# Performance work log

Hardware: AMD Instinct MI355X
Metric: run time of the kernel (lower is better)

Reference implementation:

```python
import jax, jax.numpy as jnp
import numpy as np

B, SEQ_LEN, PRED_LEN, LABEL_LEN, PERIOD, N_CH = 32, 2048, 1024, 512, 256, 256
K = SEQ_LEN // PERIOD   # seg_num_x = 8
L = PRED_LEN // PERIOD  # seg_num_y = 4
EPS = 1e-5


def setup_inputs() -> dict:
    key = jax.random.key(0)
    k1, k2, k3, k4, k5, k6, k7 = jax.random.split(key, 7)
    x_enc = jax.random.normal(k1, (B, SEQ_LEN, N_CH), jnp.float32)
    x_mark_enc = jax.random.normal(k2, (B, SEQ_LEN, 4), jnp.float32)
    x_dec = jax.random.normal(k3, (B, LABEL_LEN + PRED_LEN, N_CH), jnp.float32)
    x_mark_dec = jax.random.normal(k4, (B, LABEL_LEN + PRED_LEN, 4), jnp.float32)
    # base_model abstracted as a linear map on the time axis of a [B, PERIOD, N] segment.
    # Scaled ~1/sqrt(P) so repeated powers (up to K+L-1 = 11) stay numerically tame.
    W_base = jax.random.normal(k5, (PERIOD, PERIOD), jnp.float32) * (0.9 / np.sqrt(PERIOD))
    # new_encoders[j]: nn.Linear(seg_num_x, 1) -> weight row [K] + bias scalar per j.
    W_enc = jax.random.normal(k6, (L, K), jnp.float32) * (1.0 / np.sqrt(K))
    b_enc = jax.random.normal(k7, (L,), jnp.float32) * 0.01
    return {"x_enc": x_enc, "x_mark_enc": x_mark_enc, "x_dec": x_dec,
            "x_mark_dec": x_mark_dec, "W_base": W_base, "W_enc": W_enc, "b_enc": b_enc}


def reference(x_enc, x_mark_enc, x_dec, x_mark_dec, W_base, W_enc, b_enc):
    Bv, S, N = x_enc.shape
    # per-series normalization over time (means is .detach()'d in torch; fwd math identical)
    means = jnp.mean(x_enc, axis=1, keepdims=True)                  # [B,1,N]
    xc = x_enc - means
    stdev = jnp.sqrt(jnp.var(xc, axis=1, keepdims=True) + EPS)      # [B,1,N]
    xn = xc / stdev

    # split into K segments of length PERIOD: [K, B, P, N]
    segs = xn.reshape(Bv, K, PERIOD, N).transpose(1, 0, 2, 3)

    # x_res[l][k] = base_model applied (K - k + l) times to segment k.
    # base(x) = einsum('qp,bpn->bqn', W_base, x), so m applications = W_base^m.
    def step(c, _):
        nxt = W_base @ c
        return nxt, nxt
    _, rest = jax.lax.scan(step, W_base, None, length=K + L - 2)
    powers = jnp.concatenate([W_base[None], rest], axis=0)          # powers[i] = W^(i+1)

    exps = (K - jnp.arange(K))[None, :] + jnp.arange(L)[:, None]    # [L,K]
    Wlk = powers[exps - 1]                                          # [L,K,P,P]
    x_res = jnp.einsum('lkqp,kbpn->lkbqn', Wlk, segs)               # [L,K,B,P,N]

    # dec_out_part[l] = sum_k W_enc[l,k] * x_res[l][k] + b_enc[l] * ones
    dec = jnp.einsum('lk,lkbqn->lbqn', W_enc, x_res) + b_enc[:, None, None, None]
    dec = dec.transpose(1, 0, 2, 3).reshape(Bv, L * PERIOD, N)      # cat over time

    # de-normalize
    dec = dec * stdev[:, 0, :][:, None, :] + means[:, 0, :][:, None, :]
    return dec[:, -PRED_LEN:, :]
```

## Files before the change

### kernel.cpp

```cpp
#include <hip/hip_runtime.h>
#include <cstdint>
#include <cstddef>


typedef unsigned short ushort_t;
typedef unsigned int uint_t;
typedef __attribute__((ext_vector_type(8))) short bf16x8;
typedef __attribute__((ext_vector_type(16))) float f32x16;

__device__ __forceinline__ ushort_t f32_to_bf16(float f) {
    uint_t u = __float_as_uint(f);
    u += 0x7FFFu + ((u >> 16) & 1u);
    return (ushort_t)(u >> 16);
}
__device__ __forceinline__ float bf16_to_f32(ushort_t h) {
    return __uint_as_float((uint_t)h << 16);
}

struct PowOps { int sa[4]; int sb[4]; int sd[4]; };

__global__ void powmul(const float* __restrict__ Wb, float* __restrict__ Pw, PowOps ops) {
    __shared__ float As[4 * 256];
    const int mat = blockIdx.x;
    const int r0  = blockIdx.y * 4;
    const int tid = threadIdx.x;
    const float* A  = (ops.sa[mat] < 0) ? Wb : Pw + (size_t)ops.sa[mat] * 65536;
    const float* Bm = (ops.sb[mat] < 0) ? Wb : Pw + (size_t)ops.sb[mat] * 65536;
    float* C        = Pw + (size_t)ops.sd[mat] * 65536;
#pragma unroll
    for (int i = 0; i < 4; ++i) As[i * 256 + tid] = A[(size_t)(r0 + i) * 256 + tid];
    __syncthreads();
    float a0 = 0.f, a1 = 0.f, a2 = 0.f, a3 = 0.f;
    for (int p = 0; p < 256; p += 8) {
        float bv[8];
#pragma unroll
        for (int u = 0; u < 8; ++u) bv[u] = Bm[(size_t)(p + u) * 256 + tid];
#pragma unroll
        for (int u = 0; u < 8; ++u) {
            a0 += As[0 * 256 + p + u] * bv[u];
            a1 += As[1 * 256 + p + u] * bv[u];
            a2 += As[2 * 256 + p + u] * bv[u];
            a3 += As[3 * 256 + p + u] * bv[u];
        }
    }
    C[(size_t)(r0 + 0) * 256 + tid] = a0;
    C[(size_t)(r0 + 1) * 256 + tid] = a1;
    C[(size_t)(r0 + 2) * 256 + tid] = a2;
    C[(size_t)(r0 + 3) * 256 + tid] = a3;
}

__global__ void prep(const float* __restrict__ x, ushort_t* __restrict__ Xt,
                     float* __restrict__ ps1, float* __restrict__ ps2,
                     const float* __restrict__ Pw, const float* __restrict__ Wb,
                     const float* __restrict__ Wenc,
                     ushort_t* __restrict__ Ah, float* __restrict__ rsA) {
    __shared__ float lds[64 * 65];
    __shared__ float red1[16 * 64];
    __shared__ float red2[16 * 64];
    const int bid = blockIdx.x;
    const int tid = threadIdx.x;
    if (bid < 4096) {
        const int st = bid & 31;
        const int nt = (bid >> 5) & 3;
        const int b  = bid >> 7;
        const int c = tid & 15, r = tid >> 4;
        const int s0 = st * 64;
        float s1[4] = {0,0,0,0}, s2[4] = {0,0,0,0};
#pragma unroll
        for (int it = 0; it < 4; ++it) {
            const int ii = r + it * 16;
            const float4 v = *(const float4*)(x + ((size_t)b * 2048 + s0 + ii) * 256 + nt * 64 + c * 4);
            const float vv[4] = {v.x, v.y, v.z, v.w};
#pragma unroll
            for (int jj = 0; jj < 4; ++jj) {
                lds[ii * 65 + c * 4 + jj] = vv[jj];
                s1[jj] += vv[jj]; s2[jj] += vv[jj] * vv[jj];
            }
        }
#pragma unroll
        for (int jj = 0; jj < 4; ++jj) { red1[r * 64 + c * 4 + jj] = s1[jj]; red2[r * 64 + c * 4 + jj] = s2[jj]; }
        __syncthreads();
        if (tid < 64) {
            float a = 0.f, q = 0.f;
#pragma unroll
            for (int rr = 0; rr < 16; ++rr) { a += red1[rr * 64 + tid]; q += red2[rr * 64 + tid]; }
            const size_t o = (size_t)st * 8192 + b * 256 + nt * 64 + tid;
            ps1[o] = a; ps2[o] = q;
        }
#pragma unroll
        for (int step = 0; step < 8; ++step) {
            const int npr = step * 8 + (tid >> 5);
            const int sp  = (tid & 31) * 2;
            const float f0 = lds[sp * 65 + npr];
            const float f1 = lds[(sp + 1) * 65 + npr];
            const uint_t packed = (uint_t)f32_to_bf16(f0) | ((uint_t)f32_to_bf16(f1) << 16);
            *(uint_t*)(Xt + ((size_t)b * 256 + nt * 64 + npr) * 2048 + s0 + sp) = packed;
        }
    } else {
        const int t = bid - 4096;
        const int l = t >> 8, q = t & 255;
        const int c = tid;
        float part = 0.f;
#pragma unroll
        for (int k = 0; k < 8; ++k) {
            const int m = 8 - k + l;
            const float* src = (m == 1) ? Wb : (Pw + (size_t)(m - 2) * 65536);
            const float val = Wenc[l * 8 + k] * src[q * 256 + c];
            const ushort_t h = f32_to_bf16(val);
            Ah[(size_t)t * 2048 + k * 256 + c] = h;
            part += bf16_to_f32(h);
        }
#pragma unroll
        for (int off = 32; off > 0; off >>= 1) part += __shfl_xor(part, off);
        if ((c & 63) == 0) red1[c >> 6] = part;
        __syncthreads();
        if (c == 0) rsA[t] = red1[0] + red1[1] + red1[2] + red1[3];
    }
}

#define GLOAD_LDS16(gsrc, ldst) \
    __builtin_amdgcn_global_load_lds((const __attribute__((address_space(1))) void*)(gsrc), \
                                     (__attribute__((address_space(3))) void*)(ldst), 16, 0, 0)

__global__ __launch_bounds__(256, 2) void gemm_kernel(
    const ushort_t* __restrict__ Ah,
    const ushort_t* __restrict__ Xt,
    const float* __restrict__ ps1, const float* __restrict__ ps2,
    const float* __restrict__ rsA, const float* __restrict__ benc,
    float* __restrict__ out)
{
    __shared__ ushort_t sA[3][4096];
    __shared__ ushort_t sX[3][4096];

    const int flat = blockIdx.x;
    const int xcd  = flat & 7;
    const int j    = flat >> 3;
    const int bx   = xcd + ((j & 7) << 3);
    const int by   = j >> 3;
    const int l    = by >> 1;

    const int tid  = threadIdx.x;
    const int lane = tid & 63;
    const int w    = tid >> 6;
    const int wm   = w >> 1, wn = w & 1;
    const int li   = lane & 31, lg = lane >> 5;
    const int lq3  = (li >> 1) & 3;

    const int lrow = 2 * (lane >> 3) + ((lane >> 2) & 1);
    const int kc   = (lane & 3) ^ ((lane >> 3) & 3);
    const ushort_t* aBase0 = Ah + (size_t)(by * 128 + 16 * (2 * w + 0) + lrow) * 2048 + kc * 8;
    const ushort_t* aBase1 = Ah + (size_t)(by * 128 + 16 * (2 * w + 1) + lrow) * 2048 + kc * 8;
    const ushort_t* xBase0 = Xt + (size_t)(bx * 128 + 16 * (2 * w + 0) + lrow) * 2048 + kc * 8;
    const ushort_t* xBase1 = Xt + (size_t)(bx * 128 + 16 * (2 * w + 1) + lrow) * 2048 + kc * 8;

    ushort_t* sAf = &sA[0][0];
    ushort_t* sXf = &sX[0][0];

#define STAGE(dst_off, ko_) do { \
    GLOAD_LDS16(aBase0 + (ko_), sAf + (dst_off) + (2 * w + 0) * 512); \
    GLOAD_LDS16(aBase1 + (ko_), sAf + (dst_off) + (2 * w + 1) * 512); \
    GLOAD_LDS16(xBase0 + (ko_), sXf + (dst_off) + (2 * w + 0) * 512); \
    GLOAD_LDS16(xBase1 + (ko_), sXf + (dst_off) + (2 * w + 1) * 512); \
} while (0)

    f32x16 acc[2][2];
#pragma unroll
    for (int mm = 0; mm < 2; ++mm)
#pragma unroll
        for (int nn = 0; nn < 2; ++nn)
#pragma unroll
            for (int rr = 0; rr < 16; ++rr) acc[mm][nn][rr] = 0.0f;

    STAGE(0, 0);
    STAGE(4096, 32);

    int cb = 0;
#pragma unroll 1
    for (int kt = 0; kt < 64; ++kt) {
        if (kt < 63) { asm volatile("s_waitcnt vmcnt(4)" ::: "memory"); }
        else         { asm volatile("s_waitcnt vmcnt(0)" ::: "memory"); }
        __builtin_amdgcn_s_barrier();
        asm volatile("" ::: "memory");

        const ushort_t* pa = sAf + cb * 4096;
        const ushort_t* px = sXf + cb * 4096;
        bf16x8 af[2][2], xf[2][2];
#pragma unroll
        for (int ks = 0; ks < 2; ++ks) {
            const int sl = ((ks << 1) + lg) ^ lq3;
            const int ro = (li >> 1) * 64 + (li & 1) * 32 + sl * 8;
            af[ks][0] = *(const bf16x8*)(pa + wm * 2048 + ro);
            af[ks][1] = *(const bf16x8*)(pa + wm * 2048 + 1024 + ro);
            xf[ks][0] = *(const bf16x8*)(px + wn * 2048 + ro);
            xf[ks][1] = *(const bf16x8*)(px + wn * 2048 + 1024 + ro);
        }
        if (kt < 62) {
            const int sb_ = (cb >= 1) ? cb - 1 : 2;
            STAGE(sb_ * 4096, (kt + 2) * 32);
        }
        __builtin_amdgcn_s_setprio(1);
#pragma unroll
        for (int ks = 0; ks < 2; ++ks) {
            acc[0][0] = __builtin_amdgcn_mfma_f32_32x32x16_bf16(af[ks][0], xf[ks][0], acc[0][0], 0, 0, 0);
            acc[0][1] = __builtin_amdgcn_mfma_f32_32x32x16_bf16(af[ks][0], xf[ks][1], acc[0][1], 0, 0, 0);
            acc[1][0] = __builtin_amdgcn_mfma_f32_32x32x16_bf16(af[ks][1], xf[ks][0], acc[1][0], 0, 0, 0);
            acc[1][1] = __builtin_amdgcn_mfma_f32_32x32x16_bf16(af[ks][1], xf[ks][1], acc[1][1], 0, 0, 0);
        }
        __builtin_amdgcn_s_setprio(0);
        asm volatile("" ::: "memory");
        cb = (cb == 2) ? 0 : cb + 1;
    }
#undef STAGE

    const float be = benc[l];
    float mn[2], sd[2];
#pragma unroll
    for (int nn = 0; nn < 2; ++nn) {
        const int col = bx * 128 + wn * 64 + nn * 32 + li;
        float s = 0.f, q = 0.f;
#pragma unroll
        for (int st = 0; st < 32; ++st) {
            s += ps1[(size_t)st * 8192 + col];
            q += ps2[(size_t)st * 8192 + col];
        }
        const float mean = s * (1.0f / 2048.0f);
        float var = q * (1.0f / 2048.0f) - mean * mean;
        var = fmaxf(var, 0.0f);
        mn[nn] = mean;
        sd[nn] = sqrtf(var + 1e-5f);
    }
#pragma unroll
    for (int mm = 0; mm < 2; ++mm)
#pragma unroll
        for (int nn = 0; nn < 2; ++nn) {
            const int col = bx * 128 + wn * 64 + nn * 32 + li;
            const int bq = col >> 8, nq = col & 255;
            const float ben = be * sd[nn];
#pragma unroll
            for (int rr = 0; rr < 16; ++rr) {
                const int row = by * 128 + wm * 64 + mm * 32 + ((rr & 3) + 8 * (rr >> 2) + 4 * lg);
                out[((size_t)bq * 1024 + row) * 256 + nq] =
                    acc[mm][nn][rr] + mn[nn] * (1.0f - rsA[row]) + ben;
            }
        }
}

extern "C" void kernel_launch(void* const* d_in, const int* in_sizes, int n_in,
                              void* d_out, int out_size, void* d_ws, size_t ws_size,
                              hipStream_t stream) {
    (void)in_sizes; (void)n_in; (void)out_size; (void)ws_size;
    const float* x_enc  = (const float*)d_in[0];
    const float* W_base = (const float*)d_in[4];
    const float* W_enc  = (const float*)d_in[5];
    const float* b_enc  = (const float*)d_in[6];
    float* out = (float*)d_out;

    char* ws = (char*)d_ws;
    float*    wsP   = (float*)(ws);
    float*    wsRsA = (float*)(ws + 0x300000);
    float*    wsS1  = (float*)(ws + 0x310000);
    float*    wsS2  = (float*)(ws + 0x410000);
    ushort_t* wsAh  = (ushort_t*)(ws + 0x510000);
    ushort_t* wsXt  = (ushort_t*)(ws + 0x910000);

    { PowOps o{{-1, 0, 0, 0}, {-1, 0, 0, 0}, {0, 0, 0, 0}};
      powmul<<<dim3(1, 64), 256, 0, stream>>>(W_base, wsP, o); }
    { PowOps o{{0, 0, 0, 0}, {-1, 0, 0, 0}, {1, 2, 0, 0}};
      powmul<<<dim3(2, 64), 256, 0, stream>>>(W_base, wsP, o); }
    { PowOps o{{2, 2, 2, 2}, {-1, 0, 1, 2}, {3, 4, 5, 6}};
      powmul<<<dim3(4, 64), 256, 0, stream>>>(W_base, wsP, o); }
    { PowOps o{{6, 6, 6, 0}, {-1, 0, 1, 0}, {7, 8, 9, 0}};
      powmul<<<dim3(3, 64), 256, 0, stream>>>(W_base, wsP, o); }

    prep<<<5120, 256, 0, stream>>>(x_enc, wsXt, wsS1, wsS2, wsP, W_base, W_enc,
                                   wsAh, wsRsA);

    gemm_kernel<<<512, 256, 0, stream>>>(wsAh, wsXt, wsS1, wsS2, wsRsA, b_enc, out);
}
```

Baseline: 106.8 us.

## Factor weight powers to shrink the GEMM reduction and add a combine stage

The single large GEMM (reduction length 2048 over all segments) is replaced with a factored form W^(8-k+l) = W^l · W^(8-k). First V_k = W^(8-k)·x_k is computed per segment, then a combine kernel mixes the V_k with W_enc per output segment, and a second GEMM applies W^l (identity for l=0). This cuts total MAC work by about 2.7x and drops the highest matrix-power launch. In exchange it writes and re-reads large bf16 intermediates, adds a kernel launch, and rounds to bf16 two extra times, which risks accuracy. Mean/std finalisation and the row-sum correction move into extra blocks of the first GEMM.

```diff
diff --git a/kernel.cpp b/kernel.cpp
--- a/kernel.cpp
+++ b/kernel.cpp
@@ -52,8 +52,7 @@
 __global__ void prep(const float* __restrict__ x, ushort_t* __restrict__ Xt,
                      float* __restrict__ ps1, float* __restrict__ ps2,
                      const float* __restrict__ Pw, const float* __restrict__ Wb,
-                     const float* __restrict__ Wenc,
-                     ushort_t* __restrict__ Ah, float* __restrict__ rsA) {
+                     ushort_t* __restrict__ Pb, float* __restrict__ prs) {
     __shared__ float lds[64 * 65];
     __shared__ float red1[16 * 64];
     __shared__ float red2[16 * 64];
@@ -97,24 +96,42 @@
             *(uint_t*)(Xt + ((size_t)b * 256 + nt * 64 + npr) * 2048 + s0 + sp) = packed;
         }
     } else {
-        const int t = bid - 4096;
-        const int l = t >> 8, q = t & 255;
-        const int c = tid;
-        float part = 0.f;
-#pragma unroll
-        for (int k = 0; k < 8; ++k) {
-            const int m = 8 - k + l;
-            const float* src = (m == 1) ? Wb : (Pw + (size_t)(m - 2) * 65536);
-            const float val = Wenc[l * 8 + k] * src[q * 256 + c];
-            const ushort_t h = f32_to_bf16(val);
-            Ah[(size_t)t * 2048 + k * 256 + c] = h;
-            part += bf16_to_f32(h);
-        }
-#pragma unroll
-        for (int off = 32; off > 0; off >>= 1) part += __shfl_xor(part, off);
-        if ((c & 63) == 0) red1[c >> 6] = part;
-        __syncthreads();
-        if (c == 0) rsA[t] = red1[0] + red1[1] + red1[2] + red1[3];
+        const int ib = bid - 4096;
+        const int e  = ib >> 2;
+        const int rq = ib & 3;
+        const int q  = rq * 64 + (tid >> 2);
+        const int cc = tid & 3;
+        uint2* dst = (uint2*)(Pb + (size_t)e * 65536 + q * 256 + cc * 64);
+        float s = 0.f;
+        if (e == 0) {
+#pragma unroll
+            for (int i = 0; i < 16; ++i) {
+                uint2 o; o.x = 0u; o.y = 0u;
+                const int col0 = cc * 64 + i * 4;
+                if (q >= col0 && q < col0 + 4) {
+                    const int j = q - col0;
+                    if (j == 0) o.x = 0x3F80u; else if (j == 1) o.x = 0x3F800000u;
+                    else if (j == 2) o.y = 0x3F80u; else o.y = 0x3F800000u;
+                }
+                dst[i] = o;
+            }
+            s = 1.0f;
+        } else {
+            const float* src = (e == 1) ? Wb : (Pw + (size_t)(e - 2) * 65536);
+            const float4* sp = (const float4*)(src + (size_t)q * 256 + cc * 64);
+#pragma unroll
+            for (int i = 0; i < 16; ++i) {
+                const float4 v = sp[i];
+                const ushort_t h0 = f32_to_bf16(v.x), h1 = f32_to_bf16(v.y);
+                const ushort_t h2 = f32_to_bf16(v.z), h3 = f32_to_bf16(v.w);
+                s += bf16_to_f32(h0) + bf16_to_f32(h1) + bf16_to_f32(h2) + bf16_to_f32(h3);
+                uint2 o; o.x = (uint_t)h0 | ((uint_t)h1 << 16); o.y = (uint_t)h2 | ((uint_t)h3 << 16);
+                dst[i] = o;
+            }
+        }
+        s += __shfl_xor(s, 1);
+        s += __shfl_xor(s, 2);
+        if (cc == 0) prs[e * 256 + q] = s;
     }
 }
 
@@ -122,22 +139,191 @@
     __builtin_amdgcn_global_load_lds((const __attribute__((address_space(1))) void*)(gsrc), \
                                      (__attribute__((address_space(3))) void*)(ldst), 16, 0, 0)
 
-__global__ __launch_bounds__(256, 2) void gemm_kernel(
-    const ushort_t* __restrict__ Ah,
+__global__ __launch_bounds__(256, 2) void gemm_v(
+    const ushort_t* __restrict__ Pb,
     const ushort_t* __restrict__ Xt,
+    ushort_t* __restrict__ vt,
     const float* __restrict__ ps1, const float* __restrict__ ps2,
+    const float* __restrict__ prs, const float* __restrict__ Wenc,
+    float* __restrict__ meanv, float* __restrict__ stdv, float* __restrict__ rsA)
+{
+    __shared__ ushort_t sAa[3][4096];
+    __shared__ ushort_t sBb[3][8192];
+
+    const int bid = blockIdx.x;
+    const int tid = threadIdx.x;
+    if (bid >= 512) {
+        const int idx = bid - 512;
+        if (idx < 32) {
+            const int b = idx;
+            float s = 0.f, q = 0.f;
+#pragma unroll
+            for (int st = 0; st < 32; ++st) {
+                s += ps1[(size_t)st * 8192 + b * 256 + tid];
+                q += ps2[(size_t)st * 8192 + b * 256 + tid];
+            }
+            const float mean = s * (1.0f / 2048.0f);
+            float var = q * (1.0f / 2048.0f) - mean * mean;
+            var = fmaxf(var, 0.0f);
+            meanv[b * 256 + tid] = mean;
+            stdv [b * 256 + tid] = sqrtf(var + 1e-5f);
+        } else {
+            const int l = idx - 32;
+            float u = 0.f;
+#pragma unroll
+            for (int k = 0; k < 8; ++k) u += Wenc[l * 8 + k] * prs[(8 - k) * 256 + tid];
+            float* uf = (float*)&sAa[0][0];
+            uf[tid] = u;
+            __syncthreads();
+            const uint2* rp = (const uint2*)(Pb + (size_t)l * 65536 + tid * 256);
+            float s = 0.f;
+#pragma unroll
+            for (int i = 0; i < 64; ++i) {
+                const uint2 v = rp[i];
+                s += bf16_to_f32((ushort_t)(v.x & 0xffff)) * uf[i * 4 + 0]
+                   + bf16_to_f32((ushort_t)(v.x >> 16))    * uf[i * 4 + 1]
+                   + bf16_to_f32((ushort_t)(v.y & 0xffff)) * uf[i * 4 + 2]
+                   + bf16_to_f32((ushort_t)(v.y >> 16))    * uf[i * 4 + 3];
+            }
+            rsA[l * 256 + tid] = s;
+        }
+        return;
+    }
+
+    const int xcd  = bid & 7;
+    const int g    = bid >> 3;
+    const int colT = xcd + ((g & 7) << 3);
+    const int k    = g >> 3;
+    const int e    = 8 - k;
+
+    const int lane = tid & 63;
+    const int w    = tid >> 6;
+    const int wm   = w >> 1, wn = w & 1;
+    const int li   = lane & 31, lg = lane >> 5;
+    const int lq3  = (li >> 1) & 3;
+    const int lrow = 2 * (lane >> 3) + ((lane >> 2) & 1);
+    const int kc   = (lane & 3) ^ ((lane >> 3) & 3);
+
+    const ushort_t* xtb = Xt + (size_t)(colT * 128) * 2048 + k * 256;
+    const ushort_t* pbb = Pb + (size_t)e * 65536;
+
+#define VSTAGE(bf_, kt_) do { \
+    const int p0_ = (kt_) * 32 + kc * 8; \
+    GLOAD_LDS16(xtb + (size_t)(w * 32 + 0  + lrow) * 2048 + p0_, &sAa[bf_][(w * 32 + 0)  * 32]); \
+    GLOAD_LDS16(xtb + (size_t)(w * 32 + 16 + lrow) * 2048 + p0_, &sAa[bf_][(w * 32 + 16) * 32]); \
+    GLOAD_LDS16(pbb + (w * 64 + 0  + lrow) * 256 + p0_, &sBb[bf_][(w * 64 + 0)  * 32]); \
+    GLOAD_LDS16(pbb + (w * 64 + 16 + lrow) * 256 + p0_, &sBb[bf_][(w * 64 + 16) * 32]); \
+    GLOAD_LDS16(pbb + (w * 64 + 32 + lrow) * 256 + p0_, &sBb[bf_][(w * 64 + 32) * 32]); \
+    GLOAD_LDS16(pbb + (w * 64 + 48 + lrow) * 256 + p0_, &sBb[bf_][(w * 64 + 48) * 32]); \
+} while (0)
+
+    f32x16 acc[2][4];
+#pragma unroll
+    for (int mm = 0; mm < 2; ++mm)
+#pragma unroll
+        for (int nn = 0; nn < 4; ++nn)
+#pragma unroll
+            for (int rr = 0; rr < 16; ++rr) acc[mm][nn][rr] = 0.0f;
+
+    VSTAGE(0, 0);
+    VSTAGE(1, 1);
+
+#define VKT(kt_) do { \
+    if ((kt_) < 7) { asm volatile("s_waitcnt vmcnt(6)" ::: "memory"); } \
+    else           { asm volatile("s_waitcnt vmcnt(0)" ::: "memory"); } \
+    __builtin_amdgcn_s_barrier(); \
+    asm volatile("" ::: "memory"); \
+    const ushort_t* pa_ = &sAa[(kt_) % 3][0]; \
+    const ushort_t* px_ = &sBb[(kt_) % 3][0]; \
+    bf16x8 af[2][2], xf[2][4]; \
+    _Pragma("unroll") \
+    for (int ks = 0; ks < 2; ++ks) { \
+        const int sl = ((ks << 1) + lg) ^ lq3; \
+        const int ro = (li >> 1) * 64 + (li & 1) * 32 + sl * 8; \
+        af[ks][0] = *(const bf16x8*)(pa_ + wm * 2048 + ro); \
+        af[ks][1] = *(const bf16x8*)(pa_ + wm * 2048 + 1024 + ro); \
+        xf[ks][0] = *(const bf16x8*)(px_ + wn * 4096 + ro); \
+        xf[ks][1] = *(const bf16x8*)(px_ + wn * 4096 + 1024 + ro); \
+        xf[ks][2] = *(const bf16x8*)(px_ + wn * 4096 + 2048 + ro); \
+        xf[ks][3] = *(const bf16x8*)(px_ + wn * 4096 + 3072 + ro); \
+    } \
+    if ((kt_) < 6) { VSTAGE(((kt_) + 2) % 3, (kt_) + 2); } \
+    __builtin_amdgcn_s_setprio(1); \
+    _Pragma("unroll") \
+    for (int ks = 0; ks < 2; ++ks) \
+        _Pragma("unroll") \
+        for (int mm = 0; mm < 2; ++mm) \
+            _Pragma("unroll") \
+            for (int nn = 0; nn < 4; ++nn) \
+                acc[mm][nn] = __builtin_amdgcn_mfma_f32_32x32x16_bf16(af[ks][mm], xf[ks][nn], acc[mm][nn], 0, 0, 0); \
+    __builtin_amdgcn_s_setprio(0); \
+    asm volatile("" ::: "memory"); \
+} while (0)
+
+    VKT(0); VKT(1); VKT(2); VKT(3); VKT(4); VKT(5); VKT(6); VKT(7);
+#undef VKT
+#undef VSTAGE
+
+    ushort_t* vb = vt + (size_t)k * 2097152;
+#pragma unroll
+    for (int mm = 0; mm < 2; ++mm)
+#pragma unroll
+        for (int nn = 0; nn < 4; ++nn) {
+            const int q = wn * 128 + nn * 32 + li;
+#pragma unroll
+            for (int rr = 0; rr < 16; ++rr) {
+                const int c = colT * 128 + wm * 64 + mm * 32 + ((rr & 3) + 8 * (rr >> 2) + 4 * lg);
+                vb[(size_t)c * 256 + q] = f32_to_bf16(acc[mm][nn][rr]);
+            }
+        }
+}
+
+__global__ void combine(const ushort_t* __restrict__ vt, const float* __restrict__ Wenc,
+                        ushort_t* __restrict__ c) {
+    const int t   = threadIdx.x;
+    const int col = blockIdx.x * 8 + (t >> 5);
+    const size_t off = (size_t)col * 256 + (t & 31) * 8;
+    float a0[8] = {0,0,0,0,0,0,0,0}, a1[8] = {0,0,0,0,0,0,0,0};
+    float a2[8] = {0,0,0,0,0,0,0,0}, a3[8] = {0,0,0,0,0,0,0,0};
+#pragma unroll
+    for (int k = 0; k < 8; ++k) {
+        const bf16x8 v = *(const bf16x8*)(vt + (size_t)k * 2097152 + off);
+        const float w0 = Wenc[0 * 8 + k], w1 = Wenc[1 * 8 + k];
+        const float w2 = Wenc[2 * 8 + k], w3 = Wenc[3 * 8 + k];
+#pragma unroll
+        for (int j = 0; j < 8; ++j) {
+            const float f = bf16_to_f32((ushort_t)v[j]);
+            a0[j] += w0 * f; a1[j] += w1 * f; a2[j] += w2 * f; a3[j] += w3 * f;
+        }
+    }
+    bf16x8 o0, o1, o2, o3;
+#pragma unroll
+    for (int j = 0; j < 8; ++j) {
+        o0[j] = (short)f32_to_bf16(a0[j]); o1[j] = (short)f32_to_bf16(a1[j]);
+        o2[j] = (short)f32_to_bf16(a2[j]); o3[j] = (short)f32_to_bf16(a3[j]);
+    }
+    *(bf16x8*)(c + 0 * 2097152 + off) = o0;
+    *(bf16x8*)(c + 1 * 2097152 + off) = o1;
+    *(bf16x8*)(c + 2 * 2097152 + off) = o2;
+    *(bf16x8*)(c + 3 * 2097152 + off) = o3;
+}
+
+__global__ __launch_bounds__(256, 2) void gemm2(
+    const ushort_t* __restrict__ Pb, const ushort_t* __restrict__ c,
+    const float* __restrict__ meanv, const float* __restrict__ stdv,
     const float* __restrict__ rsA, const float* __restrict__ benc,
     float* __restrict__ out)
 {
-    __shared__ ushort_t sA[3][4096];
-    __shared__ ushort_t sX[3][4096];
-
-    const int flat = blockIdx.x;
-    const int xcd  = flat & 7;
-    const int j    = flat >> 3;
-    const int bx   = xcd + ((j & 7) << 3);
-    const int by   = j >> 3;
-    const int l    = by >> 1;
+    __shared__ ushort_t sAa[3][4096];
+    __shared__ ushort_t sBb[3][4096];
+
+    const int bid  = blockIdx.x;
+    const int xcd  = bid & 7;
+    const int g    = bid >> 3;
+    const int colT = xcd + ((g & 7) << 3);
+    const int rest = g >> 3;
+    const int l    = rest >> 1;
+    const int qpT  = rest & 1;
 
     const int tid  = threadIdx.x;
     const int lane = tid & 63;
@@ -145,22 +331,18 @@
     const int wm   = w >> 1, wn = w & 1;
     const int li   = lane & 31, lg = lane >> 5;
     const int lq3  = (li >> 1) & 3;
-
     const int lrow = 2 * (lane >> 3) + ((lane >> 2) & 1);
     const int kc   = (lane & 3) ^ ((lane >> 3) & 3);
-    const ushort_t* aBase0 = Ah + (size_t)(by * 128 + 16 * (2 * w + 0) + lrow) * 2048 + kc * 8;
-    const ushort_t* aBase1 = Ah + (size_t)(by * 128 + 16 * (2 * w + 1) + lrow) * 2048 + kc * 8;
-    const ushort_t* xBase0 = Xt + (size_t)(bx * 128 + 16 * (2 * w + 0) + lrow) * 2048 + kc * 8;
-    const ushort_t* xBase1 = Xt + (size_t)(bx * 128 + 16 * (2 * w + 1) + lrow) * 2048 + kc * 8;
-
-    ushort_t* sAf = &sA[0][0];
-    ushort_t* sXf = &sX[0][0];
-
-#define STAGE(dst_off, ko_) do { \
-    GLOAD_LDS16(aBase0 + (ko_), sAf + (dst_off) + (2 * w + 0) * 512); \
-    GLOAD_LDS16(aBase1 + (ko_), sAf + (dst_off) + (2 * w + 1) * 512); \
-    GLOAD_LDS16(xBase0 + (ko_), sXf + (dst_off) + (2 * w + 0) * 512); \
-    GLOAD_LDS16(xBase1 + (ko_), sXf + (dst_off) + (2 * w + 1) * 512); \
+
+    const ushort_t* ab = Pb + (size_t)l * 65536 + (size_t)(qpT * 128) * 256;
+    const ushort_t* cb = c + ((size_t)l * 8192 + colT * 128) * 256;
+
+#define GSTAGE(bf_, kt_) do { \
+    const int p0_ = (kt_) * 32 + kc * 8; \
+    GLOAD_LDS16(ab + (w * 32 + 0  + lrow) * 256 + p0_, &sAa[bf_][(w * 32 + 0)  * 32]); \
+    GLOAD_LDS16(ab + (w * 32 + 16 + lrow) * 256 + p0_, &sAa[bf_][(w * 32 + 16) * 32]); \
+    GLOAD_LDS16(cb + (w * 32 + 0  + lrow) * 256 + p0_, &sBb[bf_][(w * 32 + 0)  * 32]); \
+    GLOAD_LDS16(cb + (w * 32 + 16 + lrow) * 256 + p0_, &sBb[bf_][(w * 32 + 16) * 32]); \
 } while (0)
 
     f32x16 acc[2][2];
@@ -171,76 +353,64 @@
 #pragma unroll
             for (int rr = 0; rr < 16; ++rr) acc[mm][nn][rr] = 0.0f;
 
-    STAGE(0, 0);
-    STAGE(4096, 32);
-
-    int cb = 0;
-#pragma unroll 1
-    for (int kt = 0; kt < 64; ++kt) {
-        if (kt < 63) { asm volatile("s_waitcnt vmcnt(4)" ::: "memory"); }
-        else         { asm volatile("s_waitcnt vmcnt(0)" ::: "memory"); }
-        __builtin_amdgcn_s_barrier();
-        asm volatile("" ::: "memory");
-
-        const ushort_t* pa = sAf + cb * 4096;
-        const ushort_t* px = sXf + cb * 4096;
-        bf16x8 af[2][2], xf[2][2];
-#pragma unroll
-        for (int ks = 0; ks < 2; ++ks) {
-            const int sl = ((ks << 1) + lg) ^ lq3;
-            const int ro = (li >> 1) * 64 + (li & 1) * 32 + sl * 8;
-            af[ks][0] = *(const bf16x8*)(pa + wm * 2048 + ro);
-            af[ks][1] = *(const bf16x8*)(pa + wm * 2048 + 1024 + ro);
-            xf[ks][0] = *(const bf16x8*)(px + wn * 2048 + ro);
-            xf[ks][1] = *(const bf16x8*)(px + wn * 2048 + 1024 + ro);
-        }
-        if (kt < 62) {
-            const int sb_ = (cb >= 1) ? cb - 1 : 2;
-            STAGE(sb_ * 4096, (kt + 2) * 32);
-        }
-        __builtin_amdgcn_s_setprio(1);
-#pragma unroll
-        for (int ks = 0; ks < 2; ++ks) {
-            acc[0][0] = __builtin_amdgcn_mfma_f32_32x32x16_bf16(af[ks][0], xf[ks][0], acc[0][0], 0, 0, 0);
-            acc[0][1] = __builtin_amdgcn_mfma_f32_32x32x16_bf16(af[ks][0], xf[ks][1], acc[0][1], 0, 0, 0);
-            acc[1][0] = __builtin_amdgcn_mfma_f32_32x32x16_bf16(af[ks][1], xf[ks][0], acc[1][0], 0, 0, 0);
-            acc[1][1] = __builtin_amdgcn_mfma_f32_32x32x16_bf16(af[ks][1], xf[ks][1], acc[1][1], 0, 0, 0);
-        }
-        __builtin_amdgcn_s_setprio(0);
-        asm volatile("" ::: "memory");
-        cb = (cb == 2) ? 0 : cb + 1;
-    }
-#undef STAGE
+    GSTAGE(0, 0);
+    GSTAGE(1, 1);
+
+#define GKT(kt_) do { \
+    if ((kt_) < 7) { asm volatile("s_waitcnt vmcnt(4)" ::: "memory"); } \
+    else           { asm volatile("s_waitcnt vmcnt(0)" ::: "memory"); } \
+    __builtin_amdgcn_s_barrier(); \
+    asm volatile("" ::: "memory"); \
+    const ushort_t* pa_ = &sAa[(kt_) % 3][0]; \
+    const ushort_t* px_ = &sBb[(kt_) % 3][0]; \
+    bf16x8 af[2][2], xf[2][2]; \
+    _Pragma("unroll") \
+    for (int ks = 0; ks < 2; ++ks) { \
+        const int sl = ((ks << 1) + lg) ^ lq3; \
+        const int ro = (li >> 1) * 64 + (li & 1) * 32 + sl * 8; \
+        af[ks][0] = *(const bf16x8*)(pa_ + wm * 2048 + ro); \
+        af[ks][1] = *(const bf16x8*)(pa_ + wm * 2048 + 1024 + ro); \
+        xf[ks][0] = *(const bf16x8*)(px_ + wn * 2048 + ro); \
+        xf[ks][1] = *(const bf16x8*)(px_ + wn * 2048 + 1024 + ro); \
+    } \
+    if ((kt_) < 6) { GSTAGE(((kt_) + 2) % 3, (kt_) + 2); } \
+    __builtin_amdgcn_s_setprio(1); \
+    _Pragma("unroll") \
+    for (int ks = 0; ks < 2; ++ks) { \
+        acc[0][0] = __builtin_amdgcn_mfma_f32_32x32x16_bf16(af[ks][0], xf[ks][0], acc[0][0], 0, 0, 0); \
+        acc[0][1] = __builtin_amdgcn_mfma_f32_32x32x16_bf16(af[ks][0], xf[ks][1], acc[0][1], 0, 0, 0); \
+        acc[1][0] = __builtin_amdgcn_mfma_f32_32x32x16_bf16(af[ks][1], xf[ks][0], acc[1][0], 0, 0, 0); \
+        acc[1][1] = __builtin_amdgcn_mfma_f32_32x32x16_bf16(af[ks][1], xf[ks][1], acc[1][1], 0, 0, 0); \
+    } \
+    __builtin_amdgcn_s_setprio(0); \
+    asm volatile("" ::: "memory"); \
+} while (0)
+
+    GKT(0); GKT(1); GKT(2); GKT(3); GKT(4); GKT(5); GKT(6); GKT(7);
+#undef GKT
+#undef GSTAGE
 
     const float be = benc[l];
     float mn[2], sd[2];
 #pragma unroll
     for (int nn = 0; nn < 2; ++nn) {
-        const int col = bx * 128 + wn * 64 + nn * 32 + li;
-        float s = 0.f, q = 0.f;
-#pragma unroll
-        for (int st = 0; st < 32; ++st) {
-            s += ps1[(size_t)st * 8192 + col];
-            q += ps2[(size_t)st * 8192 + col];
-        }
-        const float mean = s * (1.0f / 2048.0f);
-        float var = q * (1.0f / 2048.0f) - mean * mean;
-        var = fmaxf(var, 0.0f);
-        mn[nn] = mean;
-        sd[nn] = sqrtf(var + 1e-5f);
+        const int col = colT * 128 + wn * 64 + nn * 32 + li;
+        mn[nn] = meanv[col];
+        sd[nn] = stdv [col];
     }
 #pragma unroll
     for (int mm = 0; mm < 2; ++mm)
 #pragma unroll
         for (int nn = 0; nn < 2; ++nn) {
-            const int col = bx * 128 + wn * 64 + nn * 32 + li;
+            const int col = colT * 128 + wn * 64 + nn * 32 + li;
             const int bq = col >> 8, nq = col & 255;
             const float ben = be * sd[nn];
 #pragma unroll
             for (int rr = 0; rr < 16; ++rr) {
-                const int row = by * 128 + wm * 64 + mm * 32 + ((rr & 3) + 8 * (rr >> 2) + 4 * lg);
-                out[((size_t)bq * 1024 + row) * 256 + nq] =
-                    acc[mm][nn][rr] + mn[nn] * (1.0f - rsA[row]) + ben;
+                const int trow = l * 256 + qpT * 128 + wm * 64 + mm * 32
+                               + ((rr & 3) + 8 * (rr >> 2) + 4 * lg);
+                out[((size_t)bq * 1024 + trow) * 256 + nq] =
+                    acc[mm][nn][rr] + mn[nn] * (1.0f - rsA[trow]) + ben;
             }
         }
 }
@@ -256,12 +426,17 @@
     float* out = (float*)d_out;
 
     char* ws = (char*)d_ws;
-    float*    wsP   = (float*)(ws);
-    float*    wsRsA = (float*)(ws + 0x300000);
-    float*    wsS1  = (float*)(ws + 0x310000);
-    float*    wsS2  = (float*)(ws + 0x410000);
-    ushort_t* wsAh  = (ushort_t*)(ws + 0x510000);
-    ushort_t* wsXt  = (ushort_t*)(ws + 0x910000);
+    float*    wsP    = (float*)(ws);
+    ushort_t* wsPb   = (ushort_t*)(ws + 0x200000);
+    float*    wsPrs  = (float*)(ws + 0x320000);
+    float*    wsS1   = (float*)(ws + 0x330000);
+    float*    wsS2   = (float*)(ws + 0x430000);
+    float*    wsMean = (float*)(ws + 0x530000);
+    float*    wsStd  = (float*)(ws + 0x540000);
+    float*    wsRsA  = (float*)(ws + 0x550000);
+    ushort_t* wsXt   = (ushort_t*)(ws + 0x600000);
+    ushort_t* wsC    = (ushort_t*)(ws + 0x600000);
+    ushort_t* wsVt   = (ushort_t*)(ws + 0x2600000);
 
     { PowOps o{{-1, 0, 0, 0}, {-1, 0, 0, 0}, {0, 0, 0, 0}};
       powmul<<<dim3(1, 64), 256, 0, stream>>>(W_base, wsP, o); }
@@ -269,11 +444,13 @@
       powmul<<<dim3(2, 64), 256, 0, stream>>>(W_base, wsP, o); }
     { PowOps o{{2, 2, 2, 2}, {-1, 0, 1, 2}, {3, 4, 5, 6}};
       powmul<<<dim3(4, 64), 256, 0, stream>>>(W_base, wsP, o); }
-    { PowOps o{{6, 6, 6, 0}, {-1, 0, 1, 0}, {7, 8, 9, 0}};
-      powmul<<<dim3(3, 64), 256, 0, stream>>>(W_base, wsP, o); }
-
-    prep<<<5120, 256, 0, stream>>>(x_enc, wsXt, wsS1, wsS2, wsP, W_base, W_enc,
-                                   wsAh, wsRsA);
-
-    gemm_kernel<<<512, 256, 0, stream>>>(wsAh, wsXt, wsS1, wsS2, wsRsA, b_enc, out);
-}
+
+    prep<<<4132, 256, 0, stream>>>(x_enc, wsXt, wsS1, wsS2, wsP, W_base, wsPb, wsPrs);
+
+    gemm_v<<<548, 256, 0, stream>>>(wsPb, wsXt, wsVt, wsS1, wsS2, wsPrs, W_enc,
+                                    wsMean, wsStd, wsRsA);
+
+    combine<<<1024, 256, 0, stream>>>(wsVt, W_enc, wsC);
+
+    gemm2<<<512, 256, 0, stream>>>(wsPb, wsC, wsMean, wsStd, wsRsA, b_enc, out);
+}
```

After: 98.77 us. 1.08x faster.
